# Performance work log

Hardware: AMD Instinct MI355X
Metric: run time of the kernel (lower is better)

## Reference

```python
import jax, jax.numpy as jnp
import numpy as np

D_MODEL = 1024
NUM_HEADS = 16
DEPTH = D_MODEL // NUM_HEADS
MAX_SEQ = 2048
B, S = 2, 2048


def setup_inputs() -> dict:
    key = jax.random.key(0)
    ks = jax.random.split(key, 12)
    scale = 1.0 / np.sqrt(D_MODEL)
    inp = {
        'q': jax.random.normal(ks[0], (B, S, D_MODEL), jnp.float32),
        'k': jax.random.normal(ks[1], (B, S, D_MODEL), jnp.float32),
        'v': jax.random.normal(ks[2], (B, S, D_MODEL), jnp.float32),
        'mask': jnp.zeros((B, 1, S, S), jnp.float32),
        'wq_w': jax.random.normal(ks[3], (D_MODEL, D_MODEL), jnp.float32) * scale,
        'wq_b': jnp.zeros((D_MODEL,), jnp.float32),
        'wk_w': jax.random.normal(ks[4], (D_MODEL, D_MODEL), jnp.float32) * scale,
        'wk_b': jnp.zeros((D_MODEL,), jnp.float32),
        'wv_w': jax.random.normal(ks[5], (D_MODEL, D_MODEL), jnp.float32) * scale,
        'wv_b': jnp.zeros((D_MODEL,), jnp.float32),
        'dense_w': jax.random.normal(ks[6], (D_MODEL, D_MODEL), jnp.float32) * scale,
        'dense_b': jnp.zeros((D_MODEL,), jnp.float32),
        'rel_bias': jax.random.normal(ks[7], (2 * MAX_SEQ - 1, NUM_HEADS), jnp.float32),
    }
    return inp


def _split_heads(x):
    # [B, S, D_MODEL] -> [B, H, S, depth]
    b, s, _ = x.shape
    return x.reshape(b, s, NUM_HEADS, DEPTH).transpose(0, 2, 1, 3)


def reference(q, k, v, mask, wq_w, wq_b, wk_w, wk_b, wv_w, wv_b, dense_w, dense_b, rel_bias):
    b, s, _ = q.shape
    # torch Linear: y = x @ W.T + b
    qh = _split_heads(q @ wq_w.T + wq_b)
    kh = _split_heads(k @ wk_w.T + wk_b)
    vh = _split_heads(v @ wv_w.T + wv_b)
    logits = jnp.einsum('bhqd,bhkd->bhqk', qh, kh) / jnp.sqrt(jnp.float32(DEPTH))
    # relative position bias gather
    pos = jnp.arange(s)
    idx = jnp.clip(pos[:, None] - pos[None, :] + MAX_SEQ - 1, 0, 2 * MAX_SEQ - 2)  # [S, S]
    pos_bias = rel_bias[idx]                      # [S, S, H]
    pos_bias = pos_bias.transpose(2, 0, 1)[None]  # [1, H, S, S]
    logits = logits + pos_bias + mask * (-1e9)
    attn = jax.nn.softmax(logits, axis=-1)        # dropout is identity in eval
    out = jnp.einsum('bhqk,bhkd->bhqd', attn, vh)
    out = out.transpose(0, 2, 1, 3).reshape(b, s, D_MODEL)
    out = out @ dense_w.T + dense_b
    return out, attn
```

## Files before the change

### kernel.cpp

```cpp
#include <hip/hip_runtime.h>

typedef _Float16 f16x8 __attribute__((ext_vector_type(8)));
typedef _Float16 f16x4 __attribute__((ext_vector_type(4)));
typedef float f32x4 __attribute__((ext_vector_type(4)));
typedef unsigned short u16x8 __attribute__((ext_vector_type(8)));
typedef unsigned int u32;

#define MFMA16H(a, b, c) __builtin_amdgcn_mfma_f32_16x16x32_f16(a, b, c, 0, 0, 0)

#if __has_builtin(__builtin_amdgcn_exp2f)
#define EXP2F(x) __builtin_amdgcn_exp2f(x)
#else
#define EXP2F(x) exp2f(x)
#endif

#define LOG2E 1.44269504088896340736f
#define SHIFT2 5.0f

__device__ __forceinline__ unsigned short f2bf(float x) {
  unsigned u = __float_as_uint(x);
  u += 0x7FFF + ((u >> 16) & 1);
  return (unsigned short)(u >> 16);
}
__device__ __forceinline__ float bf2f(unsigned short h) {
  return __uint_as_float(((unsigned)h) << 16);
}
__device__ __forceinline__ f16x8 ldh8(const _Float16* p) {
  return *reinterpret_cast<const f16x8*>(p);
}
__device__ __forceinline__ u16x8 ldu8(const unsigned short* p) {
  return *reinterpret_cast<const u16x8*>(p);
}

__global__ __launch_bounds__(256) void prep_kernel(
    const float* __restrict__ q, const float* __restrict__ k, const float* __restrict__ v,
    const float* __restrict__ wq, const float* __restrict__ wk, const float* __restrict__ wv,
    const float* __restrict__ dwt, const float* __restrict__ mask,
    _Float16* __restrict__ qf, _Float16* __restrict__ kf, _Float16* __restrict__ vf,
    _Float16* __restrict__ wqf, _Float16* __restrict__ wkf, _Float16* __restrict__ wvf,
    _Float16* __restrict__ dwf, unsigned short* __restrict__ mperm) {
  if (blockIdx.x < 2048) {
    const int blk = blockIdx.x;
    const int kt = blk & 31, bq = blk >> 5;
    const int b = bq >> 5, qt = bq & 31;
    const int lane = threadIdx.x;
    const int w = lane >> 6, lg = (lane >> 4) & 3, lr = lane & 15;
    const int q0 = qt * 64;
    const float cs = -1e9f * LOG2E;
    unsigned short vals[16];
#pragma unroll
    for (int c = 0; c < 4; ++c)
#pragma unroll
      for (int r = 0; r < 4; ++r) {
        const int qr = q0 + w * 16 + lg * 4 + r;
        const int kc = kt * 64 + c * 16 + lr;
        vals[c * 4 + r] = f2bf(mask[((size_t)b * 2048 + qr) * 2048 + kc] * cs);
      }
    uint4* out = reinterpret_cast<uint4*>(mperm) + ((size_t)blk * 256 + lane) * 2;
    out[0] = *reinterpret_cast<uint4*>(&vals[0]);
    out[1] = *reinterpret_cast<uint4*>(&vals[8]);
    return;
  }
  const int i = (blockIdx.x - 2048) * 256 + threadIdx.x;
  const int r = i >> 18;
  const int j = i & 262143;
  const float* src;
  _Float16* dst;
  int off = 0;
  if (r < 4)       { src = q;   dst = qf;  off = r * 262144; }
  else if (r < 8)  { src = k;   dst = kf;  off = (r - 4) * 262144; }
  else if (r < 12) { src = v;   dst = vf;  off = (r - 8) * 262144; }
  else if (r == 12){ src = wq;  dst = wqf; }
  else if (r == 13){ src = wk;  dst = wkf; }
  else if (r == 14){ src = wv;  dst = wvf; }
  else             { src = dwt; dst = dwf; }
  const int g = off + j;
  float4 x = reinterpret_cast<const float4*>(src)[g];
  f16x4 h;
  h[0] = (_Float16)x.x; h[1] = (_Float16)x.y;
  h[2] = (_Float16)x.z; h[3] = (_Float16)x.w;
  reinterpret_cast<f16x4*>(dst)[g] = h;
}

__device__ __forceinline__ void gemm_body(
    int t, int mode, const _Float16* __restrict__ A, const _Float16* __restrict__ B,
    const float* __restrict__ bias, _Float16* __restrict__ out_h, float* __restrict__ out_f,
    _Float16* As, _Float16* Bs) {
  const int tid = threadIdx.x;
  const int tm = t & 31, tn = t >> 5;
  const int m0 = tm * 128, n0 = tn * 128;
  const int w = tid >> 6, l = tid & 63, lg = l >> 4, lr = l & 15;
  const int wr = w >> 1, wc = w & 1;
  const int srow = tid >> 2, scol = (tid & 3) * 8;

  f32x4 acc[4][4] = {};

  for (int kt = 0; kt < 32; ++kt) {
    const int k0 = kt * 32;
    uint4 ra[2], rb[2];
#pragma unroll
    for (int it = 0; it < 2; ++it) {
      const int row = it * 64 + srow;
      ra[it] = *reinterpret_cast<const uint4*>(A + (size_t)(m0 + row) * 1024 + k0 + scol);
      rb[it] = *reinterpret_cast<const uint4*>(B + (size_t)(n0 + row) * 1024 + k0 + scol);
    }
    __syncthreads();
#pragma unroll
    for (int it = 0; it < 2; ++it) {
      const int eo = (it * 256 + tid) * 8;
      *reinterpret_cast<uint4*>(As + eo) = ra[it];
      *reinterpret_cast<uint4*>(Bs + eo) = rb[it];
    }
    __syncthreads();

    f16x8 fa[4], fb[4];
#pragma unroll
    for (int i = 0; i < 4; ++i) {
      fa[i] = ldh8(As + (wr * 64 + i * 16 + lr) * 32 + lg * 8);
      fb[i] = ldh8(Bs + (wc * 64 + i * 16 + lr) * 32 + lg * 8);
    }
#pragma unroll
    for (int i = 0; i < 4; ++i)
#pragma unroll
      for (int j = 0; j < 4; ++j)
        acc[i][j] = MFMA16H(fa[i], fb[j], acc[i][j]);
  }

#pragma unroll
  for (int i = 0; i < 4; ++i) {
    const int mrow = m0 + wr * 64 + i * 16 + lg * 4;
#pragma unroll
    for (int j = 0; j < 4; ++j) {
      const int ncol = n0 + wc * 64 + j * 16 + lr;
      const float bv = bias[ncol];
#pragma unroll
      for (int r = 0; r < 4; ++r) {
        const int m = mrow + r;
        const float v = acc[i][j][r] + bv;
        if (mode == 2) {
          out_f[(size_t)m * 1024 + ncol] = v;
        } else {
          const int bb = m >> 11, s = m & 2047, hh = ncol >> 6, d = ncol & 63;
          if (mode == 0)
            out_h[((size_t)(bb * 16 + hh) * 2048 + s) * 64 + d] = (_Float16)v;
          else
            out_h[((size_t)(bb * 16 + hh) * 64 + d) * 2048 + s] = (_Float16)v;
        }
      }
    }
  }
}

__global__ __launch_bounds__(256, 3) void proj_gemm_kernel(
    const _Float16* __restrict__ qf, const _Float16* __restrict__ kf, const _Float16* __restrict__ vf,
    const _Float16* __restrict__ wqf, const _Float16* __restrict__ wkf, const _Float16* __restrict__ wvf,
    const float* __restrict__ bq, const float* __restrict__ bk, const float* __restrict__ bv,
    _Float16* __restrict__ qhf, _Float16* __restrict__ khf, _Float16* __restrict__ vhT) {
  __shared__ __align__(16) _Float16 As[128 * 32];
  __shared__ __align__(16) _Float16 Bs[128 * 32];
  const int mode = blockIdx.x >> 8;
  const int t = blockIdx.x & 255;
  if (mode == 0)      gemm_body(t, 0, qf, wqf, bq, qhf, nullptr, As, Bs);
  else if (mode == 1) gemm_body(t, 0, kf, wkf, bk, khf, nullptr, As, Bs);
  else                gemm_body(t, 1, vf, wvf, bv, vhT, nullptr, As, Bs);
}

__global__ __launch_bounds__(256, 4) void attn_pv_kernel(
    const _Float16* __restrict__ qh, const _Float16* __restrict__ kh,
    const _Float16* __restrict__ vT,
    const float* __restrict__ rel_bias, const unsigned short* __restrict__ mperm,
    _Float16* __restrict__ o_h, _Float16* __restrict__ p16,
    float* __restrict__ scal) {
  __shared__ float rb2[2112];
  __shared__ __align__(16) _Float16 p_lds[64 * 76];

  const int bid = blockIdx.x;
  const int wg = ((bid & 7) << 7) | (bid >> 3);
  const int bh = wg >> 5, qt = wg & 31;
  const int b = bh >> 4, h = bh & 15;
  const int q0 = qt * 64;
  const int tid = threadIdx.x;
  const int w = tid >> 6, l = tid & 63, lg = l >> 4, lr = l & 15;

  for (int t = tid; t < 2111; t += 256)
    rb2[t] = rel_bias[(q0 + t) * 16 + h] * LOG2E - SHIFT2;

  const size_t bh_off = (size_t)bh * 2048 * 64;
  const _Float16* qhb = qh + bh_off;
  const _Float16* khb = kh + bh_off;
  const _Float16* vTb = vT + bh_off;
  const unsigned short* mpb =
      mperm + (((size_t)(b * 32 + qt) * 32) * 256 + tid) * 16;
  _Float16* pbh = p16 + (size_t)bh * 2048 * 2048;

  f16x8 qf[2];
  {
    const size_t qrow = (size_t)(q0 + w * 16 + lr) * 64;
    qf[0] = ldh8(qhb + qrow + lg * 8);
    qf[1] = ldh8(qhb + qrow + 32 + lg * 8);
  }
  __syncthreads();

  const int qbase = w * 16 + lg * 4;
  const float c1 = 0.125f * LOG2E;
  float sacc[4] = {0.f, 0.f, 0.f, 0.f};
  f32x4 acc_o[4] = {};

  for (int kt = 0; kt < 32; ++kt) {
    u16x8 m0v = ldu8(mpb + (size_t)kt * 4096);
    u16x8 m1v = ldu8(mpb + (size_t)kt * 4096 + 8);
#pragma unroll
    for (int c = 0; c < 4; ++c) {
      const int kc = kt * 64 + c * 16 + lr;
      const _Float16* kr = khb + (size_t)kc * 64 + lg * 8;
      f32x4 acc = {};
      acc = MFMA16H(qf[0], ldh8(kr), acc);
      acc = MFMA16H(qf[1], ldh8(kr + 32), acc);
#pragma unroll
      for (int r = 0; r < 4; ++r) {
        const float mbf = bf2f((c < 2) ? (unsigned short)m0v[(c & 1) * 4 + r]
                                       : (unsigned short)m1v[(c & 1) * 4 + r]);
        const float l2 = fmaf(acc[r], c1, rb2[qbase + r - kc + 2047]) + mbf;
        const float p = EXP2F(l2);
        sacc[r] += p;
        p_lds[(qbase + r) * 76 + c * 16 + lr] = (_Float16)p;
      }
    }
    f16x8 pf0 = ldh8(p_lds + (w * 16 + lr) * 76 + lg * 8);
    f16x8 pf1 = ldh8(p_lds + (w * 16 + lr) * 76 + 32 + lg * 8);
    _Float16* prow = pbh + (size_t)(q0 + w * 16 + lr) * 2048 + kt * 64 + lg * 8;
    *reinterpret_cast<f16x8*>(prow) = pf0;
    *reinterpret_cast<f16x8*>(prow + 32) = pf1;
#pragma unroll
    for (int n = 0; n < 4; ++n) {
      const _Float16* vr = vTb + (size_t)(n * 16 + lr) * 2048 + kt * 64 + lg * 8;
      acc_o[n] = MFMA16H(pf0, ldh8(vr), acc_o[n]);
      acc_o[n] = MFMA16H(pf1, ldh8(vr + 32), acc_o[n]);
    }
  }

  float inv_s[4];
#pragma unroll
  for (int r = 0; r < 4; ++r) {
    float s = sacc[r];
    s += __shfl_xor(s, 1);
    s += __shfl_xor(s, 2);
    s += __shfl_xor(s, 4);
    s += __shfl_xor(s, 8);
    inv_s[r] = 1.0f / s;
    if (lr == 0) scal[(size_t)bh * 2048 + q0 + qbase + r] = inv_s[r];
  }

#pragma unroll
  for (int n = 0; n < 4; ++n)
#pragma unroll
    for (int r = 0; r < 4; ++r) {
      const int qr = q0 + qbase + r;
      const int d = n * 16 + lr;
      o_h[((size_t)(b * 2048 + qr) * 16 + h) * 64 + d] = (_Float16)(acc_o[n][r] * inv_s[r]);
    }
}

__global__ __launch_bounds__(256) void tail_kernel(
    const _Float16* __restrict__ A, const _Float16* __restrict__ Bw,
    const float* __restrict__ bias, float* __restrict__ out_f,
    const _Float16* __restrict__ p16, const float* __restrict__ scal,
    float* __restrict__ attn) {
  __shared__ __align__(16) _Float16 As[128 * 32];
  __shared__ __align__(16) _Float16 Bs[128 * 32];
  if (blockIdx.x < 256) {
    gemm_body(blockIdx.x, 2, A, Bw, bias, nullptr, out_f, As, Bs);
    return;
  }
  f32x4* attnv = reinterpret_cast<f32x4*>(attn);
  const long long n8 = 16777216LL;
  const long long stride = (long long)(gridDim.x - 256) * 256;
  for (long long i = (long long)(blockIdx.x - 256) * 256 + threadIdx.x; i < n8; i += stride) {
    f16x8 p = reinterpret_cast<const f16x8*>(p16)[i];
    const float s = scal[i >> 8];
    f32x4 lo, hi;
    lo[0] = (float)p[0] * s; lo[1] = (float)p[1] * s;
    lo[2] = (float)p[2] * s; lo[3] = (float)p[3] * s;
    hi[0] = (float)p[4] * s; hi[1] = (float)p[5] * s;
    hi[2] = (float)p[6] * s; hi[3] = (float)p[7] * s;
    __builtin_nontemporal_store(lo, attnv + 2 * i);
    __builtin_nontemporal_store(hi, attnv + 2 * i + 1);
  }
}

extern "C" void kernel_launch(void* const* d_in, const int* in_sizes, int n_in,
                              void* d_out, int out_size, void* d_ws, size_t ws_size,
                              hipStream_t stream) {
  const float* q = (const float*)d_in[0];
  const float* k = (const float*)d_in[1];
  const float* v = (const float*)d_in[2];
  const float* mask = (const float*)d_in[3];
  const float* wq_w = (const float*)d_in[4];
  const float* wq_b = (const float*)d_in[5];
  const float* wk_w = (const float*)d_in[6];
  const float* wk_b = (const float*)d_in[7];
  const float* wv_w = (const float*)d_in[8];
  const float* wv_b = (const float*)d_in[9];
  const float* dw = (const float*)d_in[10];
  const float* db = (const float*)d_in[11];
  const float* rel = (const float*)d_in[12];

  char* ws = (char*)d_ws;
  _Float16* qf_in = (_Float16*)(ws + 0);
  _Float16* kf_in = (_Float16*)(ws + 8388608);
  _Float16* vf_in = (_Float16*)(ws + 16777216);
  _Float16* wqf   = (_Float16*)(ws + 25165824);
  _Float16* wkf   = (_Float16*)(ws + 27262976);
  _Float16* wvf   = (_Float16*)(ws + 29360128);
  _Float16* dwf   = (_Float16*)(ws + 31457280);
  _Float16* qhf   = (_Float16*)(ws + 33554432);
  _Float16* khf   = (_Float16*)(ws + 41943040);
  _Float16* vhT   = (_Float16*)(ws + 50331648);
  _Float16* o_h   = (_Float16*)(ws + 58720256);
  float* scal     = (float*)(ws + 67108864);
  unsigned short* mperm = (unsigned short*)(ws + 67371008);
  _Float16* p16   = (_Float16*)(ws + 84148224);

  float* out = (float*)d_out;
  float* attn_out = out + 4194304;

  prep_kernel<<<18432, 256, 0, stream>>>(q, k, v, wq_w, wk_w, wv_w, dw, mask,
                                         qf_in, kf_in, vf_in, wqf, wkf, wvf, dwf, mperm);

  proj_gemm_kernel<<<768, 256, 0, stream>>>(qf_in, kf_in, vf_in, wqf, wkf, wvf,
                                            wq_b, wk_b, wv_b, qhf, khf, vhT);

  attn_pv_kernel<<<1024, 256, 0, stream>>>(qhf, khf, vhT, rel, mperm, o_h, p16, scal);

  tail_kernel<<<2304, 256, 0, stream>>>(o_h, dwf, db, out, p16, scal, attn_out);
}
```

Before: 626.6 us.

## Split attention into QK and PV passes, fuse attn normalization into PV

The fused QK+PV kernel is split into a QK/exp pass and a second pass that reads the stored unnormalized probabilities. That second pass does the PV matmul and writes the normalized fp32 attention matrix in the same step. The intermediate fp16 probabilities are now stored in a fragment-native, fully coalesced per-thread layout rather than row-major. The separate attn-scaling sweep in the tail kernel goes away and the dense GEMM becomes its own launch. The change trades an extra kernel launch and a PV pass that is no longer overlapped with QK for removing the standalone elementwise pass and its strided p16 writes.

```diff
diff --git a/kernel.cpp b/kernel.cpp
--- a/kernel.cpp
+++ b/kernel.cpp
@@ -16,6 +16,8 @@
 
 #define LOG2E 1.44269504088896340736f
 #define SHIFT2 5.0f
+
+union F16U { _Float16 h; unsigned short u; };
 
 __device__ __forceinline__ unsigned short f2bf(float x) {
   unsigned u = __float_as_uint(x);
@@ -165,14 +167,94 @@
   else                gemm_body(t, 1, vf, wvf, bv, vhT, nullptr, As, Bs);
 }
 
-__global__ __launch_bounds__(256, 4) void attn_pv_kernel(
+__global__ __launch_bounds__(256) void dense_gemm_kernel(
+    const _Float16* __restrict__ A, const _Float16* __restrict__ Bw,
+    const float* __restrict__ bias, float* __restrict__ out_f) {
+  __shared__ __align__(16) _Float16 As[128 * 32];
+  __shared__ __align__(16) _Float16 Bs[128 * 32];
+  gemm_body(blockIdx.x, 2, A, Bw, bias, nullptr, out_f, As, Bs);
+}
+
+__global__ __launch_bounds__(256) void attn_qk_kernel(
     const _Float16* __restrict__ qh, const _Float16* __restrict__ kh,
-    const _Float16* __restrict__ vT,
     const float* __restrict__ rel_bias, const unsigned short* __restrict__ mperm,
-    _Float16* __restrict__ o_h, _Float16* __restrict__ p16,
-    float* __restrict__ scal) {
+    _Float16* __restrict__ p16, float* __restrict__ scal) {
   __shared__ float rb2[2112];
-  __shared__ __align__(16) _Float16 p_lds[64 * 76];
+
+  const int bid = blockIdx.x;
+  const int wg = ((bid & 7) << 7) | (bid >> 3);
+  const int bh = wg >> 5, qt = wg & 31;
+  const int h = bh & 15;
+  const int q0 = qt * 64;
+  const int tid = threadIdx.x;
+  const int w = tid >> 6, l = tid & 63, lg = l >> 4, lr = l & 15;
+
+  for (int t = tid; t < 2111; t += 256)
+    rb2[t] = rel_bias[(q0 + t) * 16 + h] * LOG2E - SHIFT2;
+
+  const size_t bh_off = (size_t)bh * 2048 * 64;
+  const _Float16* qhb = qh + bh_off;
+  const _Float16* khb = kh + bh_off;
+  const int b = bh >> 4;
+  const unsigned short* mpb =
+      mperm + (((size_t)(b * 32 + qt) * 32) * 256 + tid) * 16;
+  _Float16* pdst0 = p16 + (((size_t)(bh * 32 + qt) * 32) * 4096 + (size_t)tid * 16);
+
+  f16x8 qf[2];
+  {
+    const size_t qrow = (size_t)(q0 + w * 16 + lr) * 64;
+    qf[0] = ldh8(qhb + qrow + lg * 8);
+    qf[1] = ldh8(qhb + qrow + 32 + lg * 8);
+  }
+  __syncthreads();
+
+  const int qbase = w * 16 + lg * 4;
+  const float c1 = 0.125f * LOG2E;
+  float sacc[4] = {0.f, 0.f, 0.f, 0.f};
+
+  for (int kt = 0; kt < 32; ++kt) {
+    u16x8 m0v = ldu8(mpb + (size_t)kt * 4096);
+    u16x8 m1v = ldu8(mpb + (size_t)kt * 4096 + 8);
+    unsigned short vals[16];
+#pragma unroll
+    for (int c = 0; c < 4; ++c) {
+      const int kc = kt * 64 + c * 16 + lr;
+      const _Float16* kr = khb + (size_t)kc * 64 + lg * 8;
+      f32x4 acc = {};
+      acc = MFMA16H(qf[0], ldh8(kr), acc);
+      acc = MFMA16H(qf[1], ldh8(kr + 32), acc);
+#pragma unroll
+      for (int r = 0; r < 4; ++r) {
+        const float mbf = bf2f((c < 2) ? (unsigned short)m0v[(c & 1) * 4 + r]
+                                       : (unsigned short)m1v[(c & 1) * 4 + r]);
+        const float l2 = fmaf(acc[r], c1, rb2[qbase + r - kc + 2047]) + mbf;
+        const float p = EXP2F(l2);
+        sacc[r] += p;
+        F16U cv; cv.h = (_Float16)p;
+        vals[c * 4 + r] = cv.u;
+      }
+    }
+    uint4* pv = reinterpret_cast<uint4*>(pdst0 + (size_t)kt * 4096);
+    pv[0] = *reinterpret_cast<uint4*>(&vals[0]);
+    pv[1] = *reinterpret_cast<uint4*>(&vals[8]);
+  }
+
+#pragma unroll
+  for (int r = 0; r < 4; ++r) {
+    float s = sacc[r];
+    s += __shfl_xor(s, 1);
+    s += __shfl_xor(s, 2);
+    s += __shfl_xor(s, 4);
+    s += __shfl_xor(s, 8);
+    if (lr == 0) scal[(size_t)bh * 2048 + q0 + qbase + r] = 1.0f / s;
+  }
+}
+
+__global__ __launch_bounds__(256) void attn_pv_write_kernel(
+    const _Float16* __restrict__ vT, const _Float16* __restrict__ p16,
+    const float* __restrict__ scal, float* __restrict__ attn_out,
+    _Float16* __restrict__ o_h) {
+  __shared__ __align__(16) _Float16 p_tile[64 * 76];
 
   const int bid = blockIdx.x;
   const int wg = ((bid & 7) << 7) | (bid >> 3);
@@ -181,74 +263,69 @@
   const int q0 = qt * 64;
   const int tid = threadIdx.x;
   const int w = tid >> 6, l = tid & 63, lg = l >> 4, lr = l & 15;
-
-  for (int t = tid; t < 2111; t += 256)
-    rb2[t] = rel_bias[(q0 + t) * 16 + h] * LOG2E - SHIFT2;
+  const int qbase = w * 16 + lg * 4;
+  const int srow = w * 16 + (l >> 2);
+  const int scb = (l & 3) * 16;
 
   const size_t bh_off = (size_t)bh * 2048 * 64;
-  const _Float16* qhb = qh + bh_off;
-  const _Float16* khb = kh + bh_off;
   const _Float16* vTb = vT + bh_off;
-  const unsigned short* mpb =
-      mperm + (((size_t)(b * 32 + qt) * 32) * 256 + tid) * 16;
-  _Float16* pbh = p16 + (size_t)bh * 2048 * 2048;
-
-  f16x8 qf[2];
+  const _Float16* psrc0 = p16 + (((size_t)(bh * 32 + qt) * 32) * 4096 + (size_t)tid * 16);
+  float* attn_bh = attn_out + (size_t)bh * 2048 * 2048;
+
+  float4 inv4 = *reinterpret_cast<const float4*>(scal + (size_t)bh * 2048 + q0 + qbase);
+  const float invs[4] = {inv4.x, inv4.y, inv4.z, inv4.w};
+  const float invr = scal[(size_t)bh * 2048 + q0 + srow];
+
+  f32x4 acc_o[4] = {};
+
+  uint4 pa0, pb0, pa1, pb1;
   {
-    const size_t qrow = (size_t)(q0 + w * 16 + lr) * 64;
-    qf[0] = ldh8(qhb + qrow + lg * 8);
-    qf[1] = ldh8(qhb + qrow + 32 + lg * 8);
-  }
-  __syncthreads();
-
-  const int qbase = w * 16 + lg * 4;
-  const float c1 = 0.125f * LOG2E;
-  float sacc[4] = {0.f, 0.f, 0.f, 0.f};
-  f32x4 acc_o[4] = {};
-
-  for (int kt = 0; kt < 32; ++kt) {
-    u16x8 m0v = ldu8(mpb + (size_t)kt * 4096);
-    u16x8 m1v = ldu8(mpb + (size_t)kt * 4096 + 8);
-#pragma unroll
-    for (int c = 0; c < 4; ++c) {
-      const int kc = kt * 64 + c * 16 + lr;
-      const _Float16* kr = khb + (size_t)kc * 64 + lg * 8;
-      f32x4 acc = {};
-      acc = MFMA16H(qf[0], ldh8(kr), acc);
-      acc = MFMA16H(qf[1], ldh8(kr + 32), acc);
+    const uint4* ps = reinterpret_cast<const uint4*>(psrc0);
+    pa0 = ps[0]; pb0 = ps[1];
+  }
+
+  auto process = [&](int kt, uint4 pa, uint4 pb) {
+    unsigned short vals[16];
+    *reinterpret_cast<uint4*>(&vals[0]) = pa;
+    *reinterpret_cast<uint4*>(&vals[8]) = pb;
+#pragma unroll
+    for (int c = 0; c < 4; ++c)
 #pragma unroll
       for (int r = 0; r < 4; ++r) {
-        const float mbf = bf2f((c < 2) ? (unsigned short)m0v[(c & 1) * 4 + r]
-                                       : (unsigned short)m1v[(c & 1) * 4 + r]);
-        const float l2 = fmaf(acc[r], c1, rb2[qbase + r - kc + 2047]) + mbf;
-        const float p = EXP2F(l2);
-        sacc[r] += p;
-        p_lds[(qbase + r) * 76 + c * 16 + lr] = (_Float16)p;
+        F16U cv; cv.u = vals[c * 4 + r];
+        p_tile[(qbase + r) * 76 + c * 16 + lr] = cv.h;
       }
-    }
-    f16x8 pf0 = ldh8(p_lds + (w * 16 + lr) * 76 + lg * 8);
-    f16x8 pf1 = ldh8(p_lds + (w * 16 + lr) * 76 + 32 + lg * 8);
-    _Float16* prow = pbh + (size_t)(q0 + w * 16 + lr) * 2048 + kt * 64 + lg * 8;
-    *reinterpret_cast<f16x8*>(prow) = pf0;
-    *reinterpret_cast<f16x8*>(prow + 32) = pf1;
+    f16x8 pf0 = ldh8(p_tile + (w * 16 + lr) * 76 + lg * 8);
+    f16x8 pf1 = ldh8(p_tile + (w * 16 + lr) * 76 + 32 + lg * 8);
 #pragma unroll
     for (int n = 0; n < 4; ++n) {
       const _Float16* vr = vTb + (size_t)(n * 16 + lr) * 2048 + kt * 64 + lg * 8;
       acc_o[n] = MFMA16H(pf0, ldh8(vr), acc_o[n]);
       acc_o[n] = MFMA16H(pf1, ldh8(vr + 32), acc_o[n]);
     }
-  }
-
-  float inv_s[4];
-#pragma unroll
-  for (int r = 0; r < 4; ++r) {
-    float s = sacc[r];
-    s += __shfl_xor(s, 1);
-    s += __shfl_xor(s, 2);
-    s += __shfl_xor(s, 4);
-    s += __shfl_xor(s, 8);
-    inv_s[r] = 1.0f / s;
-    if (lr == 0) scal[(size_t)bh * 2048 + q0 + qbase + r] = inv_s[r];
+    float* arow = attn_bh + (size_t)(q0 + srow) * 2048 + kt * 64 + scb;
+#pragma unroll
+    for (int i = 0; i < 4; ++i) {
+      f16x4 pw = *reinterpret_cast<const f16x4*>(&p_tile[srow * 76 + scb + i * 4]);
+      f32x4 o;
+      o[0] = (float)pw[0] * invr; o[1] = (float)pw[1] * invr;
+      o[2] = (float)pw[2] * invr; o[3] = (float)pw[3] * invr;
+      __builtin_nontemporal_store(o, reinterpret_cast<f32x4*>(arow + i * 4));
+    }
+  };
+
+  for (int kt = 0; kt < 32; kt += 2) {
+    {
+      const uint4* ps = reinterpret_cast<const uint4*>(psrc0 + (size_t)(kt + 1) * 4096);
+      pa1 = ps[0]; pb1 = ps[1];
+    }
+    process(kt, pa0, pb0);
+    {
+      const int nk = (kt + 2) & 31;
+      const uint4* ps = reinterpret_cast<const uint4*>(psrc0 + (size_t)nk * 4096);
+      pa0 = ps[0]; pb0 = ps[1];
+    }
+    process(kt + 1, pa1, pb1);
   }
 
 #pragma unroll
@@ -257,35 +334,8 @@
     for (int r = 0; r < 4; ++r) {
       const int qr = q0 + qbase + r;
       const int d = n * 16 + lr;
-      o_h[((size_t)(b * 2048 + qr) * 16 + h) * 64 + d] = (_Float16)(acc_o[n][r] * inv_s[r]);
-    }
-}
-
-__global__ __launch_bounds__(256) void tail_kernel(
-    const _Float16* __restrict__ A, const _Float16* __restrict__ Bw,
-    const float* __restrict__ bias, float* __restrict__ out_f,
-    const _Float16* __restrict__ p16, const float* __restrict__ scal,
-    float* __restrict__ attn) {
-  __shared__ __align__(16) _Float16 As[128 * 32];
-  __shared__ __align__(16) _Float16 Bs[128 * 32];
-  if (blockIdx.x < 256) {
-    gemm_body(blockIdx.x, 2, A, Bw, bias, nullptr, out_f, As, Bs);
-    return;
-  }
-  f32x4* attnv = reinterpret_cast<f32x4*>(attn);
-  const long long n8 = 16777216LL;
-  const long long stride = (long long)(gridDim.x - 256) * 256;
-  for (long long i = (long long)(blockIdx.x - 256) * 256 + threadIdx.x; i < n8; i += stride) {
-    f16x8 p = reinterpret_cast<const f16x8*>(p16)[i];
-    const float s = scal[i >> 8];
-    f32x4 lo, hi;
-    lo[0] = (float)p[0] * s; lo[1] = (float)p[1] * s;
-    lo[2] = (float)p[2] * s; lo[3] = (float)p[3] * s;
-    hi[0] = (float)p[4] * s; hi[1] = (float)p[5] * s;
-    hi[2] = (float)p[6] * s; hi[3] = (float)p[7] * s;
-    __builtin_nontemporal_store(lo, attnv + 2 * i);
-    __builtin_nontemporal_store(hi, attnv + 2 * i + 1);
-  }
+      o_h[((size_t)(b * 2048 + qr) * 16 + h) * 64 + d] = (_Float16)(acc_o[n][r] * invs[r]);
+    }
 }
 
 extern "C" void kernel_launch(void* const* d_in, const int* in_sizes, int n_in,
@@ -330,7 +380,9 @@
   proj_gemm_kernel<<<768, 256, 0, stream>>>(qf_in, kf_in, vf_in, wqf, wkf, wvf,
                                             wq_b, wk_b, wv_b, qhf, khf, vhT);
 
-  attn_pv_kernel<<<1024, 256, 0, stream>>>(qhf, khf, vhT, rel, mperm, o_h, p16, scal);
-
-  tail_kernel<<<2304, 256, 0, stream>>>(o_h, dwf, db, out, p16, scal, attn_out);
-}
+  attn_qk_kernel<<<1024, 256, 0, stream>>>(qhf, khf, rel, mperm, p16, scal);
+
+  attn_pv_write_kernel<<<1024, 256, 0, stream>>>(vhT, p16, scal, attn_out, o_h);
+
+  dense_gemm_kernel<<<256, 256, 0, stream>>>(o_h, dwf, db, out);
+}
```

After: 1.103 ms. +76.1%, slower.

## Split attention into a row-sum pass and a normalized emit pass writing fp32 attn

Applied to the files above, without the earlier changes.

Replaces the single attention pass that staged unnormalized fp16 probabilities in a workspace buffer with two passes. The first pass recomputes QK^T only to get softmax row sums, split across two key halves. The second pass recomputes the logits, normalizes them, writes fp32 attention directly and does the PV product. This removes the fp16 round trip through global memory and the separate conversion kernel, at the cost of computing QK^T twice and adding one more launch. It also moves to 32-row tiles with 128-thread blocks and runs the output projection GEMM as its own kernel.

```diff
diff --git a/kernel.cpp b/kernel.cpp
--- a/kernel.cpp
+++ b/kernel.cpp
@@ -165,48 +165,56 @@
   else                gemm_body(t, 1, vf, wvf, bv, vhT, nullptr, As, Bs);
 }
 
-__global__ __launch_bounds__(256, 4) void attn_pv_kernel(
+__global__ __launch_bounds__(256) void dense_gemm_kernel(
+    const _Float16* __restrict__ A, const _Float16* __restrict__ Bw,
+    const float* __restrict__ bias, float* __restrict__ out_f) {
+  __shared__ __align__(16) _Float16 As[128 * 32];
+  __shared__ __align__(16) _Float16 Bs[128 * 32];
+  gemm_body(blockIdx.x, 2, A, Bw, bias, nullptr, out_f, As, Bs);
+}
+
+__global__ __launch_bounds__(128) void attn_sums_kernel(
     const _Float16* __restrict__ qh, const _Float16* __restrict__ kh,
-    const _Float16* __restrict__ vT,
     const float* __restrict__ rel_bias, const unsigned short* __restrict__ mperm,
-    _Float16* __restrict__ o_h, _Float16* __restrict__ p16,
-    float* __restrict__ scal) {
-  __shared__ float rb2[2112];
-  __shared__ __align__(16) _Float16 p_lds[64 * 76];
-
+    float* __restrict__ sums2) {
+  __shared__ float rb2[2080];
   const int bid = blockIdx.x;
-  const int wg = ((bid & 7) << 7) | (bid >> 3);
-  const int bh = wg >> 5, qt = wg & 31;
+  const int wg = ((bid & 7) << 9) | (bid >> 3);
+  const int half = wg & 1;
+  const int qt = (wg >> 1) & 63;
+  const int bh = wg >> 7;
   const int b = bh >> 4, h = bh & 15;
-  const int q0 = qt * 64;
+  const int q0 = qt * 32;
   const int tid = threadIdx.x;
-  const int w = tid >> 6, l = tid & 63, lg = l >> 4, lr = l & 15;
-
-  for (int t = tid; t < 2111; t += 256)
+  const int w2 = tid >> 6, l = tid & 63, lg = l >> 4, lr = l & 15;
+
+  for (int t = tid; t < 2079; t += 128)
     rb2[t] = rel_bias[(q0 + t) * 16 + h] * LOG2E - SHIFT2;
 
   const size_t bh_off = (size_t)bh * 2048 * 64;
   const _Float16* qhb = qh + bh_off;
   const _Float16* khb = kh + bh_off;
-  const _Float16* vTb = vT + bh_off;
+  const int qt64 = qt >> 1;
+  const int wp = (qt & 1) * 2 + w2;
+  const int lanep = wp * 64 + lg * 16 + lr;
   const unsigned short* mpb =
-      mperm + (((size_t)(b * 32 + qt) * 32) * 256 + tid) * 16;
-  _Float16* pbh = p16 + (size_t)bh * 2048 * 2048;
+      mperm + (((size_t)(b * 32 + qt64) * 32) * 256 + lanep) * 16;
 
   f16x8 qf[2];
   {
-    const size_t qrow = (size_t)(q0 + w * 16 + lr) * 64;
+    const size_t qrow = (size_t)(q0 + w2 * 16 + lr) * 64;
     qf[0] = ldh8(qhb + qrow + lg * 8);
     qf[1] = ldh8(qhb + qrow + 32 + lg * 8);
   }
   __syncthreads();
 
-  const int qbase = w * 16 + lg * 4;
+  const int qbase = w2 * 16 + lg * 4;
   const float c1 = 0.125f * LOG2E;
   float sacc[4] = {0.f, 0.f, 0.f, 0.f};
-  f32x4 acc_o[4] = {};
-
-  for (int kt = 0; kt < 32; ++kt) {
+
+  const int kt0 = half * 16;
+#pragma unroll 2
+  for (int kt = kt0; kt < kt0 + 16; ++kt) {
     u16x8 m0v = ldu8(mpb + (size_t)kt * 4096);
     u16x8 m1v = ldu8(mpb + (size_t)kt * 4096 + 8);
 #pragma unroll
@@ -221,25 +229,11 @@
         const float mbf = bf2f((c < 2) ? (unsigned short)m0v[(c & 1) * 4 + r]
                                        : (unsigned short)m1v[(c & 1) * 4 + r]);
         const float l2 = fmaf(acc[r], c1, rb2[qbase + r - kc + 2047]) + mbf;
-        const float p = EXP2F(l2);
-        sacc[r] += p;
-        p_lds[(qbase + r) * 76 + c * 16 + lr] = (_Float16)p;
+        sacc[r] += EXP2F(l2);
       }
     }
-    f16x8 pf0 = ldh8(p_lds + (w * 16 + lr) * 76 + lg * 8);
-    f16x8 pf1 = ldh8(p_lds + (w * 16 + lr) * 76 + 32 + lg * 8);
-    _Float16* prow = pbh + (size_t)(q0 + w * 16 + lr) * 2048 + kt * 64 + lg * 8;
-    *reinterpret_cast<f16x8*>(prow) = pf0;
-    *reinterpret_cast<f16x8*>(prow + 32) = pf1;
-#pragma unroll
-    for (int n = 0; n < 4; ++n) {
-      const _Float16* vr = vTb + (size_t)(n * 16 + lr) * 2048 + kt * 64 + lg * 8;
-      acc_o[n] = MFMA16H(pf0, ldh8(vr), acc_o[n]);
-      acc_o[n] = MFMA16H(pf1, ldh8(vr + 32), acc_o[n]);
-    }
-  }
-
-  float inv_s[4];
+  }
+
 #pragma unroll
   for (int r = 0; r < 4; ++r) {
     float s = sacc[r];
@@ -247,8 +241,104 @@
     s += __shfl_xor(s, 2);
     s += __shfl_xor(s, 4);
     s += __shfl_xor(s, 8);
-    inv_s[r] = 1.0f / s;
-    if (lr == 0) scal[(size_t)bh * 2048 + q0 + qbase + r] = inv_s[r];
+    if (lr == 0)
+      sums2[((size_t)bh * 2048 + q0 + qbase + r) * 2 + half] = s;
+  }
+}
+
+__global__ __launch_bounds__(128) void attn_emit_kernel(
+    const _Float16* __restrict__ qh, const _Float16* __restrict__ kh,
+    const _Float16* __restrict__ vT,
+    const float* __restrict__ rel_bias, const unsigned short* __restrict__ mperm,
+    const float* __restrict__ sums2, float* __restrict__ attn_out,
+    _Float16* __restrict__ o_h) {
+  __shared__ float rb2[2080];
+  __shared__ __align__(16) _Float16 p16t[2][32 * 76];
+
+  const int bid = blockIdx.x;
+  const int wg = ((bid & 7) << 8) | (bid >> 3);
+  const int qt = wg & 63;
+  const int bh = wg >> 6;
+  const int b = bh >> 4, h = bh & 15;
+  const int q0 = qt * 32;
+  const int tid = threadIdx.x;
+  const int w2 = tid >> 6, l = tid & 63, lg = l >> 4, lr = l & 15;
+
+  for (int t = tid; t < 2079; t += 128)
+    rb2[t] = rel_bias[(q0 + t) * 16 + h] * LOG2E - SHIFT2;
+
+  const size_t bh_off = (size_t)bh * 2048 * 64;
+  const _Float16* qhb = qh + bh_off;
+  const _Float16* khb = kh + bh_off;
+  const _Float16* vTb = vT + bh_off;
+  const int qt64 = qt >> 1;
+  const int wp = (qt & 1) * 2 + w2;
+  const int lanep = wp * 64 + lg * 16 + lr;
+  const unsigned short* mpb =
+      mperm + (((size_t)(b * 32 + qt64) * 32) * 256 + lanep) * 16;
+  float* attn_bh = attn_out + (size_t)bh * 2048 * 2048;
+
+  const int qbase = w2 * 16 + lg * 4;
+
+  f16x8 qf[2];
+  {
+    const size_t qrow = (size_t)(q0 + w2 * 16 + lr) * 64;
+    qf[0] = ldh8(qhb + qrow + lg * 8);
+    qf[1] = ldh8(qhb + qrow + 32 + lg * 8);
+  }
+  float inv[4];
+  {
+    const float* sp = sums2 + ((size_t)bh * 2048 + q0 + qbase) * 2;
+    float4 s0 = *reinterpret_cast<const float4*>(sp);
+    float4 s1 = *reinterpret_cast<const float4*>(sp + 4);
+    inv[0] = 1.0f / (s0.x + s0.y);
+    inv[1] = 1.0f / (s0.z + s0.w);
+    inv[2] = 1.0f / (s1.x + s1.y);
+    inv[3] = 1.0f / (s1.z + s1.w);
+  }
+  __syncthreads();
+
+  const float c1 = 0.125f * LOG2E;
+  f32x4 acc_o[4] = {};
+  const int sg = l >> 4, sc = (l & 15) * 4;
+
+#pragma unroll 2
+  for (int kt = 0; kt < 32; ++kt) {
+    _Float16* tile = p16t[kt & 1];
+    u16x8 m0v = ldu8(mpb + (size_t)kt * 4096);
+    u16x8 m1v = ldu8(mpb + (size_t)kt * 4096 + 8);
+#pragma unroll
+    for (int c = 0; c < 4; ++c) {
+      const int kc = kt * 64 + c * 16 + lr;
+      const _Float16* kr = khb + (size_t)kc * 64 + lg * 8;
+      f32x4 acc = {};
+      acc = MFMA16H(qf[0], ldh8(kr), acc);
+      acc = MFMA16H(qf[1], ldh8(kr + 32), acc);
+#pragma unroll
+      for (int r = 0; r < 4; ++r) {
+        const float mbf = bf2f((c < 2) ? (unsigned short)m0v[(c & 1) * 4 + r]
+                                       : (unsigned short)m1v[(c & 1) * 4 + r]);
+        const float l2 = fmaf(acc[r], c1, rb2[qbase + r - kc + 2047]) + mbf;
+        tile[(qbase + r) * 76 + c * 16 + lr] = (_Float16)(EXP2F(l2) * inv[r]);
+      }
+    }
+    f16x8 pf0 = ldh8(tile + (w2 * 16 + lr) * 76 + lg * 8);
+    f16x8 pf1 = ldh8(tile + (w2 * 16 + lr) * 76 + 32 + lg * 8);
+#pragma unroll
+    for (int n = 0; n < 4; ++n) {
+      const _Float16* vr = vTb + (size_t)(n * 16 + lr) * 2048 + kt * 64 + lg * 8;
+      acc_o[n] = MFMA16H(pf0, ldh8(vr), acc_o[n]);
+      acc_o[n] = MFMA16H(pf1, ldh8(vr + 32), acc_o[n]);
+    }
+#pragma unroll
+    for (int i = 0; i < 4; ++i) {
+      const int row = w2 * 16 + i * 4 + sg;
+      f16x4 pw = *reinterpret_cast<const f16x4*>(tile + row * 76 + sc);
+      float4 o;
+      o.x = (float)pw[0]; o.y = (float)pw[1];
+      o.z = (float)pw[2]; o.w = (float)pw[3];
+      *reinterpret_cast<float4*>(attn_bh + (size_t)(q0 + row) * 2048 + kt * 64 + sc) = o;
+    }
   }
 
 #pragma unroll
@@ -257,35 +347,8 @@
     for (int r = 0; r < 4; ++r) {
       const int qr = q0 + qbase + r;
       const int d = n * 16 + lr;
-      o_h[((size_t)(b * 2048 + qr) * 16 + h) * 64 + d] = (_Float16)(acc_o[n][r] * inv_s[r]);
-    }
-}
-
-__global__ __launch_bounds__(256) void tail_kernel(
-    const _Float16* __restrict__ A, const _Float16* __restrict__ Bw,
-    const float* __restrict__ bias, float* __restrict__ out_f,
-    const _Float16* __restrict__ p16, const float* __restrict__ scal,
-    float* __restrict__ attn) {
-  __shared__ __align__(16) _Float16 As[128 * 32];
-  __shared__ __align__(16) _Float16 Bs[128 * 32];
-  if (blockIdx.x < 256) {
-    gemm_body(blockIdx.x, 2, A, Bw, bias, nullptr, out_f, As, Bs);
-    return;
-  }
-  f32x4* attnv = reinterpret_cast<f32x4*>(attn);
-  const long long n8 = 16777216LL;
-  const long long stride = (long long)(gridDim.x - 256) * 256;
-  for (long long i = (long long)(blockIdx.x - 256) * 256 + threadIdx.x; i < n8; i += stride) {
-    f16x8 p = reinterpret_cast<const f16x8*>(p16)[i];
-    const float s = scal[i >> 8];
-    f32x4 lo, hi;
-    lo[0] = (float)p[0] * s; lo[1] = (float)p[1] * s;
-    lo[2] = (float)p[2] * s; lo[3] = (float)p[3] * s;
-    hi[0] = (float)p[4] * s; hi[1] = (float)p[5] * s;
-    hi[2] = (float)p[6] * s; hi[3] = (float)p[7] * s;
-    __builtin_nontemporal_store(lo, attnv + 2 * i);
-    __builtin_nontemporal_store(hi, attnv + 2 * i + 1);
-  }
+      o_h[((size_t)(b * 2048 + qr) * 16 + h) * 64 + d] = (_Float16)acc_o[n][r];
+    }
 }
 
 extern "C" void kernel_launch(void* const* d_in, const int* in_sizes, int n_in,
@@ -317,9 +380,8 @@
   _Float16* khf   = (_Float16*)(ws + 41943040);
   _Float16* vhT   = (_Float16*)(ws + 50331648);
   _Float16* o_h   = (_Float16*)(ws + 58720256);
-  float* scal     = (float*)(ws + 67108864);
-  unsigned short* mperm = (unsigned short*)(ws + 67371008);
-  _Float16* p16   = (_Float16*)(ws + 84148224);
+  float* sums2    = (float*)(ws + 67108864);
+  unsigned short* mperm = (unsigned short*)(ws + 67633152);
 
   float* out = (float*)d_out;
   float* attn_out = out + 4194304;
@@ -330,7 +392,10 @@
   proj_gemm_kernel<<<768, 256, 0, stream>>>(qf_in, kf_in, vf_in, wqf, wkf, wvf,
                                             wq_b, wk_b, wv_b, qhf, khf, vhT);
 
-  attn_pv_kernel<<<1024, 256, 0, stream>>>(qhf, khf, vhT, rel, mperm, o_h, p16, scal);
-
-  tail_kernel<<<2304, 256, 0, stream>>>(o_h, dwf, db, out, p16, scal, attn_out);
-}
+  attn_sums_kernel<<<4096, 128, 0, stream>>>(qhf, khf, rel, mperm, sums2);
+
+  attn_emit_kernel<<<2048, 128, 0, stream>>>(qhf, khf, vhT, rel, mperm,
+                                             sums2, attn_out, o_h);
+
+  dense_gemm_kernel<<<256, 256, 0, stream>>>(o_h, dwf, db, out);
+}
```

New measurement: 681.4 us. 1.09x slower.
